# Optimization experiments

Measured on AMD Instinct MI355X. Metric: run time of the kernel, lower is better.

The kernel has to match this reference:

```python
import jax, jax.numpy as jnp
import numpy as np

B, L, H, E = 2, 2048, 16, 64  # self-attention: S=L, D=E


def setup_inputs() -> dict:
    key = jax.random.key(0)
    kq, kk, kv = jax.random.split(key, 3)
    queries = jax.random.normal(kq, (B, L, H, E), dtype=jnp.float32)
    keys = jax.random.normal(kk, (B, L, H, E), dtype=jnp.float32)
    values = jax.random.normal(kv, (B, L, H, E), dtype=jnp.float32)
    return {"queries": queries, "keys": keys, "values": values}


def reference(queries, keys, values):
    # Faithful to source: scale is computed in torch code but never applied.
    # scores: [B, H, L, S]
    scores = jnp.einsum("blhe,bshe->bhls", queries, keys)
    # TriangularCausalMask: triu(ones, diagonal=1) -> mask strictly-future positions
    Lq = queries.shape[1]
    causal = jnp.triu(jnp.ones((Lq, Lq), dtype=bool), k=1)  # [L, S]
    scores = jnp.where(causal[None, None, :, :], -jnp.inf, scores)
    A = jax.nn.softmax(scores, axis=-1)  # dropout in eval mode = identity
    V = jnp.einsum("bhls,bshd->blhd", A, values)
    return V
```

## Files before the change

kernel.cpp:

```cpp
#include <hip/hip_runtime.h>

typedef short bf16x8 __attribute__((ext_vector_type(8)));
typedef short bf16x4 __attribute__((ext_vector_type(4)));
typedef short bf16x2 __attribute__((ext_vector_type(2)));
typedef _Float16 f16x8 __attribute__((ext_vector_type(8)));
typedef float f32x4 __attribute__((ext_vector_type(4)));

#define LOG2E 1.4426950408889634f

static __device__ __forceinline__ unsigned short f2bf(float x) {
  unsigned int u = __builtin_bit_cast(unsigned int, x);
  u += 0x7fffu + ((u >> 16) & 1u);
  return (unsigned short)(u >> 16);
}
static __device__ __forceinline__ float bf2f(unsigned short h) {
  unsigned int u = ((unsigned int)h) << 16;
  return __builtin_bit_cast(float, u);
}

static __device__ __forceinline__ void gl_lds16(const void* g, void* l) {
  __builtin_amdgcn_global_load_lds(
      (const __attribute__((address_space(1))) void*)g,
      (__attribute__((address_space(3))) void*)l, 16, 0, 0);
}

__global__ __launch_bounds__(256)
void prep_kv(const float* __restrict__ K, const float* __restrict__ V,
             short* __restrict__ ws) {
  __shared__ float tmp[64 * 65];
  const int isV = blockIdx.x >> 10;
  const int tile = blockIdx.x & 1023;
  const int bh = tile >> 5, kt = tile & 31;
  const int b = bh >> 4, h = bh & 15;
  const int tid = threadIdx.x;
  if (!isV) {
    const float* Kb = K + ((size_t)b * 2048 + kt * 64) * 1024 + h * 64;
    short* okf = ws + (size_t)tile * 4096;
    for (int i = 0; i < 2; ++i) {
      const int chunk = tid + 256 * i;
      const int row = chunk >> 3, p = chunk & 7;
      const int c = p ^ (row & 7);
      const float* src = Kb + (size_t)row * 1024 + c * 8;
      const f32x4 a = *(const f32x4*)src;
      const f32x4 d = *(const f32x4*)(src + 4);
      f16x8 hk;
      for (int j = 0; j < 4; ++j) hk[j] = (_Float16)a[j];
      for (int j = 0; j < 4; ++j) hk[4 + j] = (_Float16)d[j];
      *(f16x8*)(okf + chunk * 8) = hk;
    }
  } else {
    const float* Vb = V + ((size_t)b * 2048 + kt * 64) * 1024 + h * 64;
    short* ovt = ws + 4194304 + (size_t)tile * 4096;
    for (int i = 0; i < 4; ++i) {
      const int idx = tid + 256 * i;
      const int row = idx >> 4, c4 = idx & 15;
      const f32x4 v = *(const f32x4*)(Vb + (size_t)row * 1024 + c4 * 4);
      for (int j = 0; j < 4; ++j) tmp[row * 65 + c4 * 4 + j] = v[j];
    }
    __syncthreads();
    for (int i = 0; i < 2; ++i) {
      const int chunk = tid + 256 * i;
      const int e = chunk >> 3, p = chunk & 7;
      const int s0 = (p ^ (e & 7)) * 8;
      bf16x8 o;
      for (int j = 0; j < 8; ++j) o[j] = (short)f2bf(tmp[(s0 + j) * 65 + e]);
      *(bf16x8*)(ovt + chunk * 8) = o;
    }
  }
}

__global__ __launch_bounds__(256, 4)
void fa_fwd2(const float* __restrict__ Qg, const short* __restrict__ ws,
             float* __restrict__ Og) {
  __shared__ short sKf[2][4096];
  __shared__ short sVt[2][4096];
  __shared__ short sP[4096];

  const int tid = threadIdx.x;
  const int lane = tid & 63;
  const int wv = tid >> 6;
  const int ml = lane & 15, quad = lane >> 4;
  const int bh = blockIdx.x;
  const int b = bh >> 4, h = bh & 15;
  const float* Qb = Qg + (size_t)b * 2048 * 1024 + h * 64;
  float* Ob = Og + (size_t)b * 2048 * 1024 + h * 64;
  const short* wsKf = ws;
  const short* wsVt = ws + 4194304;
  const int wrow0 = wv * 16;
  const bf16x8 ones = {16256, 16256, 16256, 16256, 16256, 16256, 16256, 16256};
  const f32x4 vzero = {0.f, 0.f, 0.f, 0.f};

  const int qt = 31 - (int)blockIdx.y;
  const int qbase = qt * 64;
  const int nkt = qt + 1;

  f16x8 qhi[2], qlo[2];
  {
    const float* qr = Qb + (size_t)(qbase + wrow0 + ml) * 1024;
    for (int ks = 0; ks < 2; ++ks) {
      const int e0 = ks * 32 + quad * 8;
      const f32x4 a = *(const f32x4*)(qr + e0);
      const f32x4 c4 = *(const f32x4*)(qr + e0 + 4);
      for (int j = 0; j < 4; ++j) {
        const float x = a[j] * LOG2E;
        const _Float16 hb = (_Float16)x;
        qhi[ks][j] = hb;
        qlo[ks][j] = (_Float16)(x - (float)hb);
      }
      for (int j = 0; j < 4; ++j) {
        const float x = c4[j] * LOG2E;
        const _Float16 hb = (_Float16)x;
        qhi[ks][4 + j] = hb;
        qlo[ks][4 + j] = (_Float16)(x - (float)hb);
      }
    }
  }

  f32x4 acc[4];
  f32x4 accl = vzero;
  for (int et = 0; et < 4; ++et) acc[et] = vzero;

  auto stage = [&](int kt, int bf) {
    const size_t ktile = ((size_t)bh * 32 + kt) * 4096;
    const short* g0 = wsKf + ktile;
    const short* g2 = wsVt + ktile;
    const int o0 = tid * 8, o1 = (tid + 256) * 8;
    gl_lds16(g0 + o0, &sKf[bf][o0]);
    gl_lds16(g0 + o1, &sKf[bf][o1]);
    gl_lds16(g2 + o0, &sVt[bf][o0]);
    gl_lds16(g2 + o1, &sVt[bf][o1]);
  };

  stage(0, 0);
  __syncthreads();

#pragma unroll 2
  for (int kt = 0; kt < nkt; ++kt) {
    const int buf = kt & 1;
    if (kt + 1 < nkt) stage(kt + 1, buf ^ 1);

    f32x4 S[4];
    for (int nt = 0; nt < 4; ++nt) S[nt] = vzero;
    for (int ks = 0; ks < 2; ++ks) {
      const int ch = (ks << 2) + quad;
      for (int nt = 0; nt < 4; ++nt) {
        const int srow = nt * 16 + ml;
        const int off = srow * 64 + ((ch ^ (srow & 7)) << 3);
        const f16x8 kh = *(const f16x8*)(&sKf[buf][off]);
        S[nt] = __builtin_amdgcn_mfma_f32_16x16x32_f16(qhi[ks], kh, S[nt], 0, 0, 0);
        S[nt] = __builtin_amdgcn_mfma_f32_16x16x32_f16(qlo[ks], kh, S[nt], 0, 0, 0);
      }
    }

    const bool dg = (kt * 64 + 63) > (qbase + wrow0);
    for (int nt = 0; nt < 4; ++nt)
      for (int r = 0; r < 4; ++r) {
        float p = __builtin_amdgcn_exp2f(S[nt][r]);
        if (dg) {
          const int sg = kt * 64 + nt * 16 + ml;
          const int lg = qbase + wrow0 + quad * 4 + r;
          if (sg > lg) p = 0.f;
        }
        const int pr = wrow0 + quad * 4 + r;
        const int s = nt * 16 + ml;
        sP[pr * 64 + (((s >> 3) ^ (pr & 7)) << 3) + (s & 7)] =
            (short)(__builtin_bit_cast(unsigned int, p) >> 16);
      }

    for (int ks = 0; ks < 2; ++ks) {
      const int ch = (ks << 2) + quad;
      const int lrow = wrow0 + ml;
      const bf16x8 pa = *(const bf16x8*)(&sP[lrow * 64 + ((ch ^ (lrow & 7)) << 3)]);
      accl = __builtin_amdgcn_mfma_f32_16x16x32_bf16(pa, ones, accl, 0, 0, 0);
      for (int et = 0; et < 4; ++et) {
        const int e = et * 16 + ml;
        const bf16x8 vb = *(const bf16x8*)(&sVt[buf][e * 64 + ((ch ^ (e & 7)) << 3)]);
        acc[et] = __builtin_amdgcn_mfma_f32_16x16x32_bf16(pa, vb, acc[et], 0, 0, 0);
      }
    }
    __syncthreads();
  }

  for (int r = 0; r < 4; ++r) {
    const float inv = 1.0f / accl[r];
    float* orow = Ob + (size_t)(qbase + wrow0 + quad * 4 + r) * 1024;
    for (int et = 0; et < 4; ++et)
      orow[et * 16 + ml] = acc[et][r] * inv;
  }
}

__global__ __launch_bounds__(512, 2)
void fa_fwd_fb(const float* __restrict__ Qg, const float* __restrict__ Kg,
               const float* __restrict__ Vg, float* __restrict__ Og) {
  constexpr int HE = 1024, Lr = 2048;
  __shared__ short sKhi[2][64 * 64];
  __shared__ short sKlo[2][64 * 64];
  __shared__ short sVt[2][64 * 64];
  __shared__ short sP[128 * 64];

  const int tid = threadIdx.x;
  const int lane = tid & 63;
  const int wv = tid >> 6;
  const int ml = lane & 15;
  const int quad = lane >> 4;

  const int b = blockIdx.x >> 4, h = blockIdx.x & 15;
  const size_t headoff = (size_t)b * (size_t)Lr * HE + (size_t)h * 64;
  const float* Qb = Qg + headoff;
  const float* Kb = Kg + headoff;
  const float* Vb = Vg + headoff;
  float* Ob = Og + headoff;

  const f32x4 vzero = {0.f, 0.f, 0.f, 0.f};

  for (int half = 0; half < 2; ++half) {
    const int qt = half ? (15 - (int)blockIdx.y) : (int)blockIdx.y;
    const int qbase = qt * 128;
    const int wrow0 = wv * 16;

    bf16x8 qhi[2], qlo[2];
    {
      const float* qr = Qb + (size_t)(qbase + wrow0 + ml) * HE;
      for (int ks = 0; ks < 2; ++ks) {
        const int e0 = ks * 32 + quad * 8;
        const f32x4 a = *(const f32x4*)(qr + e0);
        const f32x4 c4 = *(const f32x4*)(qr + e0 + 4);
        for (int j = 0; j < 4; ++j) {
          const unsigned short hb = f2bf(a[j]);
          qhi[ks][j] = (short)hb;
          qlo[ks][j] = (short)f2bf(a[j] - bf2f(hb));
        }
        for (int j = 0; j < 4; ++j) {
          const unsigned short hb = f2bf(c4[j]);
          qhi[ks][4 + j] = (short)hb;
          qlo[ks][4 + j] = (short)f2bf(c4[j] - bf2f(hb));
        }
      }
    }

    f32x4 acc[4];
    float mrun[4], lrun[4];
    for (int et = 0; et < 4; ++et) acc[et] = vzero;
    for (int r = 0; r < 4; ++r) { mrun[r] = -1e30f; lrun[r] = 0.f; }

    const int nkt = 2 * qt + 2;
    for (int kt = 0; kt < nkt; ++kt) {
      const int buf = kt & 1;
      for (int i = 0; i < 2; ++i) {
        const int idx = tid + 512 * i;
        const int row = idx >> 4, c = idx & 15;
        const f32x4 kv = *(const f32x4*)(Kb + (size_t)(kt * 64 + row) * HE + c * 4);
        bf16x4 hi, lo;
        for (int j = 0; j < 4; ++j) {
          const unsigned short hb = f2bf(kv[j]);
          hi[j] = (short)hb;
          lo[j] = (short)f2bf(kv[j] - bf2f(hb));
        }
        const int off = row * 64 + (((c >> 1) ^ (row & 7)) << 3) + ((c & 1) << 2);
        *(bf16x4*)(&sKhi[buf][off]) = hi;
        *(bf16x4*)(&sKlo[buf][off]) = lo;
      }
      {
        const int c = tid & 15, rb = tid >> 4;
        const int s0 = rb * 2;
        const f32x4 v0 = *(const f32x4*)(Vb + (size_t)(kt * 64 + s0) * HE + c * 4);
        const f32x4 v1 = *(const f32x4*)(Vb + (size_t)(kt * 64 + s0 + 1) * HE + c * 4);
        for (int j = 0; j < 4; ++j) {
          const int e = c * 4 + j;
          bf16x2 p;
          p[0] = (short)f2bf(v0[j]);
          p[1] = (short)f2bf(v1[j]);
          const int off = e * 64 + (((s0 >> 3) ^ (e & 7)) << 3) + (s0 & 7);
          *(bf16x2*)(&sVt[buf][off]) = p;
        }
      }
      __syncthreads();

      f32x4 S[4];
      for (int nt = 0; nt < 4; ++nt) S[nt] = vzero;
      for (int ks = 0; ks < 2; ++ks) {
        const int ch = (ks << 2) + quad;
        for (int nt = 0; nt < 4; ++nt) {
          const int srow = nt * 16 + ml;
          const int off = srow * 64 + ((ch ^ (srow & 7)) << 3);
          const bf16x8 kh = *(const bf16x8*)(&sKhi[buf][off]);
          const bf16x8 kl = *(const bf16x8*)(&sKlo[buf][off]);
          S[nt] = __builtin_amdgcn_mfma_f32_16x16x32_bf16(qhi[ks], kh, S[nt], 0, 0, 0);
          S[nt] = __builtin_amdgcn_mfma_f32_16x16x32_bf16(qlo[ks], kh, S[nt], 0, 0, 0);
          S[nt] = __builtin_amdgcn_mfma_f32_16x16x32_bf16(qhi[ks], kl, S[nt], 0, 0, 0);
        }
      }

      if (kt * 64 + 63 > qbase + wrow0) {
        for (int nt = 0; nt < 4; ++nt)
          for (int r = 0; r < 4; ++r) {
            const int sg = kt * 64 + nt * 16 + ml;
            const int lg = qbase + wrow0 + quad * 4 + r;
            if (sg > lg) S[nt][r] = -1e30f;
          }
      }

      float mnew[4], al[4], rsum[4];
      for (int r = 0; r < 4; ++r) {
        float mx = fmaxf(fmaxf(S[0][r], S[1][r]), fmaxf(S[2][r], S[3][r]));
        mx = fmaxf(mx, __shfl_xor(mx, 1));
        mx = fmaxf(mx, __shfl_xor(mx, 2));
        mx = fmaxf(mx, __shfl_xor(mx, 4));
        mx = fmaxf(mx, __shfl_xor(mx, 8));
        mnew[r] = fmaxf(mrun[r], mx);
        al[r] = __builtin_amdgcn_exp2f((mrun[r] - mnew[r]) * LOG2E);
        mrun[r] = mnew[r];
        rsum[r] = 0.f;
      }
      for (int nt = 0; nt < 4; ++nt)
        for (int r = 0; r < 4; ++r) {
          const float p = __builtin_amdgcn_exp2f((S[nt][r] - mnew[r]) * LOG2E);
          S[nt][r] = p;
          rsum[r] += p;
        }
      for (int r = 0; r < 4; ++r) {
        rsum[r] += __shfl_xor(rsum[r], 1);
        rsum[r] += __shfl_xor(rsum[r], 2);
        rsum[r] += __shfl_xor(rsum[r], 4);
        rsum[r] += __shfl_xor(rsum[r], 8);
        lrun[r] = lrun[r] * al[r] + rsum[r];
      }
      for (int et = 0; et < 4; ++et)
        for (int r = 0; r < 4; ++r) acc[et][r] *= al[r];

      for (int nt = 0; nt < 4; ++nt)
        for (int r = 0; r < 4; ++r) {
          const int pr = wrow0 + quad * 4 + r;
          const int s = nt * 16 + ml;
          sP[pr * 64 + (((s >> 3) ^ (pr & 7)) << 3) + (s & 7)] = (short)f2bf(S[nt][r]);
        }

      for (int ks = 0; ks < 2; ++ks) {
        const int ch = (ks << 2) + quad;
        const int lrow = wrow0 + ml;
        const bf16x8 pa = *(const bf16x8*)(&sP[lrow * 64 + ((ch ^ (lrow & 7)) << 3)]);
        for (int et = 0; et < 4; ++et) {
          const int e = et * 16 + ml;
          const bf16x8 vb = *(const bf16x8*)(&sVt[buf][e * 64 + ((ch ^ (e & 7)) << 3)]);
          acc[et] = __builtin_amdgcn_mfma_f32_16x16x32_bf16(pa, vb, acc[et], 0, 0, 0);
        }
      }
    }

    for (int r = 0; r < 4; ++r) {
      const float inv = 1.0f / lrun[r];
      float* orow = Ob + (size_t)(qbase + wrow0 + quad * 4 + r) * HE;
      for (int et = 0; et < 4; ++et)
        orow[et * 16 + ml] = acc[et][r] * inv;
    }
  }
}

extern "C" void kernel_launch(void* const* d_in, const int* in_sizes, int n_in,
                              void* d_out, int out_size, void* d_ws, size_t ws_size,
                              hipStream_t stream) {
  const float* Q = (const float*)d_in[0];
  const float* K = (const float*)d_in[1];
  const float* V = (const float*)d_in[2];
  float* O = (float*)d_out;
  if (ws_size >= 16777216u) {
    short* ws = (short*)d_ws;
    hipLaunchKernelGGL(prep_kv, dim3(2048, 1, 1), dim3(256, 1, 1), 0, stream, K, V, ws);
    hipLaunchKernelGGL(fa_fwd2, dim3(32, 32, 1), dim3(256, 1, 1), 0, stream, Q, ws, O);
  } else {
    hipLaunchKernelGGL(fa_fwd_fb, dim3(32, 8, 1), dim3(512, 1, 1), 0, stream, Q, K, V, O);
  }
}
```

Measured before the change: 132.3 us.

## Load K fragments directly into registers instead of staging through LDS

The K prep kernel now writes K tiles in MFMA fragment order, so each lane can read its operands straight from global memory into a double-buffered register array. The LDS buffer for K is removed, and the next tile's K fragments are prefetched after the QK MFMAs. This cuts LDS traffic and shared memory use, which may allow higher occupancy. In exchange it adds 64 VGPRs per thread for the fragment buffers, and every wave loads K separately from global memory or L2.

```diff
diff --git a/kernel.cpp b/kernel.cpp
--- a/kernel.cpp
+++ b/kernel.cpp
@@ -38,9 +38,11 @@
     short* okf = ws + (size_t)tile * 4096;
     for (int i = 0; i < 2; ++i) {
       const int chunk = tid + 256 * i;
-      const int row = chunk >> 3, p = chunk & 7;
-      const int c = p ^ (row & 7);
-      const float* src = Kb + (size_t)row * 1024 + c * 8;
+      const int nk = chunk >> 6, L = chunk & 63;
+      const int nt = nk >> 1, ks = nk & 1;
+      const int row = nt * 16 + (L & 15);
+      const int col = ks * 32 + (L >> 4) * 8;
+      const float* src = Kb + (size_t)row * 1024 + col;
       const f32x4 a = *(const f32x4*)src;
       const f32x4 d = *(const f32x4*)(src + 4);
       f16x8 hk;
@@ -72,7 +74,6 @@
 __global__ __launch_bounds__(256, 4)
 void fa_fwd2(const float* __restrict__ Qg, const short* __restrict__ ws,
              float* __restrict__ Og) {
-  __shared__ short sKf[2][4096];
   __shared__ short sVt[2][4096];
   __shared__ short sP[4096];
 
@@ -120,37 +121,40 @@
   f32x4 accl = vzero;
   for (int et = 0; et < 4; ++et) acc[et] = vzero;
 
-  auto stage = [&](int kt, int bf) {
-    const size_t ktile = ((size_t)bh * 32 + kt) * 4096;
-    const short* g0 = wsKf + ktile;
-    const short* g2 = wsVt + ktile;
+  f16x8 kfrag[2][8];
+  auto loadK = [&](int kt, int bf) {
+    const short* g = wsKf + ((size_t)bh * 32 + kt) * 4096;
+#pragma unroll
+    for (int i = 0; i < 8; ++i)
+      kfrag[bf][i] = *(const f16x8*)(g + (i * 64 + lane) * 8);
+  };
+
+  auto stageV = [&](int kt, int bf) {
+    const short* g2 = wsVt + ((size_t)bh * 32 + kt) * 4096;
     const int o0 = tid * 8, o1 = (tid + 256) * 8;
-    gl_lds16(g0 + o0, &sKf[bf][o0]);
-    gl_lds16(g0 + o1, &sKf[bf][o1]);
     gl_lds16(g2 + o0, &sVt[bf][o0]);
     gl_lds16(g2 + o1, &sVt[bf][o1]);
   };
 
-  stage(0, 0);
+  loadK(0, 0);
+  stageV(0, 0);
   __syncthreads();
 
 #pragma unroll 2
   for (int kt = 0; kt < nkt; ++kt) {
     const int buf = kt & 1;
-    if (kt + 1 < nkt) stage(kt + 1, buf ^ 1);
+    if (kt + 1 < nkt) stageV(kt + 1, buf ^ 1);
 
     f32x4 S[4];
     for (int nt = 0; nt < 4; ++nt) S[nt] = vzero;
-    for (int ks = 0; ks < 2; ++ks) {
-      const int ch = (ks << 2) + quad;
+    for (int ks = 0; ks < 2; ++ks)
       for (int nt = 0; nt < 4; ++nt) {
-        const int srow = nt * 16 + ml;
-        const int off = srow * 64 + ((ch ^ (srow & 7)) << 3);
-        const f16x8 kh = *(const f16x8*)(&sKf[buf][off]);
+        const f16x8 kh = kfrag[buf][nt * 2 + ks];
         S[nt] = __builtin_amdgcn_mfma_f32_16x16x32_f16(qhi[ks], kh, S[nt], 0, 0, 0);
         S[nt] = __builtin_amdgcn_mfma_f32_16x16x32_f16(qlo[ks], kh, S[nt], 0, 0, 0);
       }
-    }
+
+    if (kt + 1 < nkt) loadK(kt + 1, buf ^ 1);
 
     const bool dg = (kt * 64 + 63) > (qbase + wrow0);
     for (int nt = 0; nt < 4; ++nt)
```

Measured after the change: 290.1 us. 119% more time.
